# Performance work log

Hardware: AMD Instinct MI355X
Metric: run time of the kernel (lower is better)

Reference implementation:

```python
import jax, jax.numpy as jnp
import numpy as np

B, SQ, SK, D = 8, 4096, 4096, 64


def setup_inputs() -> dict:
    key = jax.random.key(0)
    k1, k2, k3 = jax.random.split(key, 3)
    x1 = jax.random.normal(k1, (B, SQ, D), dtype=jnp.float32)   # queries
    x2 = jax.random.normal(k2, (B, SK, D), dtype=jnp.float32)   # keys
    x3 = jax.random.normal(k3, (B, SK, D), dtype=jnp.float32)   # values
    x4 = 0                                                      # dropout p (static, 0 => deterministic)
    x5 = jnp.ones((1,), dtype=jnp.float32)                      # scale divisor
    return {"x1": x1, "x2": x2, "x3": x3, "x4": x4, "x5": x5}


def reference(x1, x2, x3, x4, x5):
    # scores: [B, Sq, Sk]
    scores = jnp.einsum("bqd,bkd->bqk", x1, x2) / x5
    attn = jax.nn.softmax(scores, axis=-1)
    p = float(x4)  # static python scalar
    if p > 0.0:
        mask = jax.random.bernoulli(jax.random.key(42), 1.0 - p, attn.shape)
        attn = attn * mask.astype(attn.dtype) / (1.0 - p)
    # out: [B, Sq, D]
    return jnp.einsum("bqk,bkd->bqd", attn, x3)
```

## Files before the change

kernel.cpp:

```cpp
#include <hip/hip_runtime.h>


typedef _Float16 f16x8 __attribute__((ext_vector_type(8)));
typedef _Float16 f16x4 __attribute__((ext_vector_type(4)));
typedef __fp16   h16x2 __attribute__((ext_vector_type(2)));
typedef float    f32x4 __attribute__((ext_vector_type(4)));
typedef float    f32x16 __attribute__((ext_vector_type(16)));

constexpr int kB  = 8;
constexpr int kSQ = 4096;
constexpr int kSK = 4096;
constexpr int kD  = 64;
constexpr int KSPLIT = 4;
constexpr int SKH = kSK / KSPLIT;
constexpr int BQ  = 128;
constexpr int MT  = 2;
constexpr int BK  = 64;
constexpr int PSTR = 72;
constexpr float kLog2e = 1.44269504088896340736f;
constexpr float kDeferThr = 11.5f;

static __device__ __forceinline__ f16x4 pack4(float a, float b, float c, float d) {
    h16x2 p0 = __builtin_amdgcn_cvt_pkrtz(a, b);
    h16x2 p1 = __builtin_amdgcn_cvt_pkrtz(c, d);
    f16x4 r;
    r[0] = (_Float16)p0[0]; r[1] = (_Float16)p0[1];
    r[2] = (_Float16)p1[0]; r[3] = (_Float16)p1[1];
    return r;
}
static __device__ __forceinline__ f16x8 pack8(const float4& a, const float4& c) {
    f16x4 lo = pack4(a.x, a.y, a.z, a.w);
    f16x4 hi = pack4(c.x, c.y, c.z, c.w);
    f16x8 f;
    f[0] = lo[0]; f[1] = lo[1]; f[2] = lo[2]; f[3] = lo[3];
    f[4] = hi[0]; f[5] = hi[1]; f[6] = hi[2]; f[7] = hi[3];
    return f;
}
static __device__ __forceinline__ unsigned pkrtz_u(float a, float b) {
    union { h16x2 h; unsigned u; } cv;
    cv.h = __builtin_amdgcn_cvt_pkrtz(a, b);
    return cv.u;
}
static __device__ __forceinline__ float xhalf_max(float x) {
    union { float f; unsigned u; } uv; uv.f = x;
    auto pr = __builtin_amdgcn_permlane32_swap(uv.u, uv.u, false, false);
    union { unsigned u; float f; } r0, r1;
    r0.u = pr[0]; r1.u = pr[1];
    return fmaxf(r0.f, r1.f);
}

typedef const __attribute__((address_space(1))) unsigned int* gu32p;
typedef __attribute__((address_space(3))) unsigned int* lu32p;
static __device__ __forceinline__ void gload_lds16(const void* g, void* l) {
    __builtin_amdgcn_global_load_lds((gu32p)g, (lu32p)l, 16, 0, 0);
}

#define PA_SLICE(dst, sv, rb) do {                                          \
    unsigned c0 = pkrtz_u((sv)[(rb)+0], (sv)[(rb)+1]);                      \
    unsigned c1 = pkrtz_u((sv)[(rb)+2], (sv)[(rb)+3]);                      \
    unsigned c2 = pkrtz_u((sv)[(rb)+4], (sv)[(rb)+5]);                      \
    unsigned c3 = pkrtz_u((sv)[(rb)+6], (sv)[(rb)+7]);                      \
    auto r02 = __builtin_amdgcn_permlane32_swap(c0, c2, false, false);      \
    auto r13 = __builtin_amdgcn_permlane32_swap(c1, c3, false, false);      \
    union { unsigned u[4]; f16x8 v; } _r;                                   \
    _r.u[0] = r02[0]; _r.u[1] = r13[0]; _r.u[2] = r02[1]; _r.u[3] = r13[1]; \
    dst = _r.v;                                                             \
} while (0)

__global__ __launch_bounds__(256, 2)
void fattn_prepass(const float* __restrict__ Kg,
                   const float* __restrict__ Vg,
                   _Float16* __restrict__ Kh,
                   _Float16* __restrict__ Vt)
{
    __shared__ _Float16 tr[kD][BK];

    const int tid = threadIdx.x;
    const int kt  = blockIdx.x;
    const int b   = blockIdx.y;

    const int k = tid >> 2;
    const int p = tid & 3;
    const int gk = kt * BK + k;

    {
        const float* src = Kg + ((size_t)b * kSK + gk) * kD + p * 16;
        const float4 a0 = *(const float4*)(src + 0);
        const float4 a1 = *(const float4*)(src + 4);
        const float4 a2 = *(const float4*)(src + 8);
        const float4 a3 = *(const float4*)(src + 12);
        _Float16* dst = Kh + ((size_t)b * kSK + gk) * kD;
        const int fb0 = 2 * p, fb1 = 2 * p + 1;
        *(f16x8*)&dst[(fb0 ^ (gk & 7)) * 8] = pack8(a0, a1);
        *(f16x8*)&dst[(fb1 ^ (gk & 7)) * 8] = pack8(a2, a3);
    }
    {
        const float* src = Vg + ((size_t)b * kSK + gk) * kD + p * 16;
        const float4 a0 = *(const float4*)(src + 0);
        const float4 a1 = *(const float4*)(src + 4);
        const float4 a2 = *(const float4*)(src + 8);
        const float4 a3 = *(const float4*)(src + 12);
        const float v[16] = {a0.x,a0.y,a0.z,a0.w, a1.x,a1.y,a1.z,a1.w,
                             a2.x,a2.y,a2.z,a2.w, a3.x,a3.y,a3.z,a3.w};
#pragma unroll
        for (int j = 0; j < 16; ++j)
            tr[p * 16 + j][k] = (_Float16)v[j];
    }
    __syncthreads();
    {
        const int f  = tid >> 2;
        const int p2 = tid & 3;
        const f16x8 b0 = *(const f16x8*)&tr[f][p2 * 16 + 0];
        const f16x8 b1 = *(const f16x8*)&tr[f][p2 * 16 + 8];
        _Float16* dst = Vt + (((size_t)b * 64 + kt) * kD + f) * BK;
        const int kb0 = 2 * p2, kb1 = 2 * p2 + 1;
        *(f16x8*)&dst[(kb0 ^ (f & 7)) * 8] = b0;
        *(f16x8*)&dst[(kb1 ^ (f & 7)) * 8] = b1;
    }
}

__global__ __launch_bounds__(512, 2)
void fattn_fused(const float* __restrict__ Qg,
                 const _Float16* __restrict__ Kh,
                 const _Float16* __restrict__ Vt,
                 const float* __restrict__ sdiv,
                 float* __restrict__ Og)
{
    __shared__ __align__(16) char smem[131072];
    _Float16* sKb = (_Float16*)smem;
    _Float16* sVb = (_Float16*)(smem + 65536);
    _Float16* sPart = (_Float16*)smem;
    float2*   sMl   = (float2*)(smem + (size_t)2 * 4 * 64 * PSTR * 2);

    const int tid  = threadIdx.x;
    const int w    = tid >> 6;
    const int lane = tid & 63;
    const int l31  = lane & 31;
    const int hi   = lane >> 5;
    const int ks   = w & 3;
    const int mh   = w >> 2;

    const int flat = blockIdx.x;
    const int b    = flat & 7;
    const int qi   = flat >> 3;
    const int qb   = qi * BQ;

    const float qscale = kLog2e / sdiv[0];

    const float* Qb = Qg + ((size_t)b * kSQ + qb) * kD;
    const _Float16* Khb = Kh + ((size_t)b * kSK + (size_t)ks * SKH) * kD;
    const _Float16* Vtb = Vt + (((size_t)b * 64 + (size_t)ks * (SKH / BK)) * kD) * BK;

    _Float16* sK = sKb + (ks * 2) * 4096;
    _Float16* sV = sVb + (ks * 2) * 4096;

    f16x8 qf[MT][4];
#pragma unroll
    for (int mt = 0; mt < MT; ++mt) {
        const float* qrow = Qb + (size_t)(mh * 64 + mt * 32 + l31) * kD;
#pragma unroll
        for (int ds = 0; ds < 4; ++ds) {
            const float4 a  = *(const float4*)(qrow + ds * 16 + hi * 8);
            const float4 cc = *(const float4*)(qrow + ds * 16 + hi * 8 + 4);
            float4 as = make_float4(a.x * qscale, a.y * qscale, a.z * qscale, a.w * qscale);
            float4 cs = make_float4(cc.x * qscale, cc.y * qscale, cc.z * qscale, cc.w * qscale);
            qf[mt][ds] = pack8(as, cs);
        }
    }

    f16x8 ones;
#pragma unroll
    for (int j = 0; j < 8; ++j) ones[j] = (_Float16)1.0f;

    int offA[4];
#pragma unroll
    for (int i = 0; i < 4; ++i)
        offA[i] = l31 * 64 + (((2 * i + hi) ^ (l31 & 7)) * 8);

    auto stage = [&](int kt, int buf) {
        const char* gk = (const char*)(Khb + (size_t)kt * BK * kD) + mh * 4096 + lane * 16;
        const char* gv = (const char*)(Vtb + (size_t)kt * kD * BK) + mh * 4096 + lane * 16;
        char* lk = (char*)&sK[buf * 4096] + mh * 4096;
        char* lv = (char*)&sV[buf * 4096] + mh * 4096;
        gload_lds16(gk,        lk);
        gload_lds16(gk + 1024, lk + 1024);
        gload_lds16(gk + 2048, lk + 2048);
        gload_lds16(gk + 3072, lk + 3072);
        gload_lds16(gv,        lv);
        gload_lds16(gv + 1024, lv + 1024);
        gload_lds16(gv + 2048, lv + 2048);
        gload_lds16(gv + 3072, lv + 3072);
    };

    f32x16 oL[MT], oH[MT];
    f32x16 ol[MT];
    float m_i[MT];
#pragma unroll
    for (int mt = 0; mt < MT; ++mt) {
        m_i[mt] = -1e30f;
#pragma unroll
        for (int r = 0; r < 16; ++r) { oL[mt][r] = 0.0f; oH[mt][r] = 0.0f; ol[mt][r] = 0.0f; }
    }

    stage(0, 0);
    __syncthreads();

    const int nIter = SKH / BK;
    for (int kt = 0; kt < nIter; ++kt) {
        const int buf = kt & 1;
        if (kt + 1 < nIter) stage(kt + 1, buf ^ 1);

        f16x8 kf0[4], kf1[4];
#pragma unroll
        for (int ds = 0; ds < 4; ++ds) {
            kf0[ds] = *(const f16x8*)&sK[buf * 4096 + offA[ds]];
            kf1[ds] = *(const f16x8*)&sK[buf * 4096 + offA[ds] + 2048];
        }

        f32x16 s0[MT], s1[MT];
#pragma unroll
        for (int mt = 0; mt < MT; ++mt)
#pragma unroll
            for (int r = 0; r < 16; ++r) { s0[mt][r] = 0.0f; s1[mt][r] = 0.0f; }

        __builtin_amdgcn_s_setprio(1);
#pragma unroll
        for (int ds = 0; ds < 4; ++ds)
#pragma unroll
            for (int mt = 0; mt < MT; ++mt) {
                s0[mt] = __builtin_amdgcn_mfma_f32_32x32x16_f16(kf0[ds], qf[mt][ds], s0[mt], 0, 0, 0);
                s1[mt] = __builtin_amdgcn_mfma_f32_32x32x16_f16(kf1[ds], qf[mt][ds], s1[mt], 0, 0, 0);
            }
        __builtin_amdgcn_s_setprio(0);

        f16x8 vf[4][2];
#pragma unroll
        for (int s = 0; s < 4; ++s) {
            vf[s][0] = *(const f16x8*)&sV[buf * 4096 + offA[s]];
            vf[s][1] = *(const f16x8*)&sV[buf * 4096 + offA[s] + 2048];
        }

#pragma unroll
        for (int mt = 0; mt < MT; ++mt) {
            float t[16];
#pragma unroll
            for (int r = 0; r < 16; ++r) t[r] = fmaxf(s0[mt][r], s1[mt][r]);
#pragma unroll
            for (int r = 0; r < 8; ++r)  t[r] = fmaxf(t[r], t[r + 8]);
#pragma unroll
            for (int r = 0; r < 4; ++r)  t[r] = fmaxf(t[r], t[r + 4]);
            float rm = fmaxf(fmaxf(t[0], t[1]), fmaxf(t[2], t[3]));
            rm = xhalf_max(rm);

            if (!__all(rm <= m_i[mt] + kDeferThr)) {
                const float mnew  = fmaxf(m_i[mt], rm);
                const float alpha = __builtin_amdgcn_exp2f(m_i[mt] - mnew);
                ol[mt][0] *= alpha;
#pragma unroll
                for (int r = 0; r < 16; ++r) { oL[mt][r] *= alpha; oH[mt][r] *= alpha; }
                m_i[mt] = mnew;
            }

#pragma unroll
            for (int r = 0; r < 16; ++r) {
                s0[mt][r] = __builtin_amdgcn_exp2f(s0[mt][r] - m_i[mt]);
                s1[mt][r] = __builtin_amdgcn_exp2f(s1[mt][r] - m_i[mt]);
            }

            f16x8 pa[4];
            PA_SLICE(pa[0], s0[mt], 0);
            PA_SLICE(pa[1], s0[mt], 8);
            PA_SLICE(pa[2], s1[mt], 0);
            PA_SLICE(pa[3], s1[mt], 8);

            __builtin_amdgcn_s_setprio(1);
#pragma unroll
            for (int s = 0; s < 4; ++s) {
                oL[mt] = __builtin_amdgcn_mfma_f32_32x32x16_f16(vf[s][0], pa[s], oL[mt], 0, 0, 0);
                oH[mt] = __builtin_amdgcn_mfma_f32_32x32x16_f16(vf[s][1], pa[s], oH[mt], 0, 0, 0);
                ol[mt] = __builtin_amdgcn_mfma_f32_32x32x16_f16(ones,     pa[s], ol[mt], 0, 0, 0);
            }
            __builtin_amdgcn_s_setprio(0);
        }

        __syncthreads();
    }

#pragma unroll
    for (int mt = 0; mt < MT; ++mt) {
        const int ql = mt * 32 + l31;
        const float lf = ol[mt][0];
        const float inv = 1.0f / lf;
        _Float16* prow = sPart + ((size_t)(mh * 4 + ks) * 64 + ql) * PSTR;
#pragma unroll
        for (int g = 0; g < 4; ++g) {
            *(f16x4*)&prow[g * 8 + hi * 4] =
                pack4(oL[mt][4 * g] * inv, oL[mt][4 * g + 1] * inv,
                      oL[mt][4 * g + 2] * inv, oL[mt][4 * g + 3] * inv);
            *(f16x4*)&prow[32 + g * 8 + hi * 4] =
                pack4(oH[mt][4 * g] * inv, oH[mt][4 * g + 1] * inv,
                      oH[mt][4 * g + 2] * inv, oH[mt][4 * g + 3] * inv);
        }
        if (hi == 0) sMl[(mh * 4 + ks) * 64 + ql] = make_float2(m_i[mt], lf);
    }
    __syncthreads();

    {
        const int qrow = tid >> 2;
        const int cc   = (tid & 3) * 16;
        const int emh  = qrow >> 6;
        const int eql  = qrow & 63;

        float2 ml[KSPLIT];
        float m = -1e30f;
#pragma unroll
        for (int s = 0; s < KSPLIT; ++s) {
            ml[s] = sMl[(emh * 4 + s) * 64 + eql];
            m = fmaxf(m, ml[s].x);
        }
        float wgt[KSPLIT];
        float lsum = 0.f;
#pragma unroll
        for (int s = 0; s < KSPLIT; ++s) {
            wgt[s] = __builtin_amdgcn_exp2f(ml[s].x - m) * ml[s].y;
            lsum += wgt[s];
        }
        const float inv = 1.0f / lsum;

        float* orow = Og + (((size_t)b * kSQ + qb + qrow)) * kD + cc;
#pragma unroll
        for (int j = 0; j < 4; ++j) {
            float a0 = 0.f, a1 = 0.f, a2 = 0.f, a3 = 0.f;
#pragma unroll
            for (int s = 0; s < KSPLIT; ++s) {
                const f16x4 a = *(const f16x4*)&sPart[((size_t)(emh * 4 + s) * 64 + eql) * PSTR + cc + j * 4];
                a0 += wgt[s] * (float)a[0];
                a1 += wgt[s] * (float)a[1];
                a2 += wgt[s] * (float)a[2];
                a3 += wgt[s] * (float)a[3];
            }
            *(float4*)&orow[j * 4] = make_float4(a0 * inv, a1 * inv, a2 * inv, a3 * inv);
        }
    }
}

extern "C" void kernel_launch(void* const* d_in, const int* in_sizes, int n_in,
                              void* d_out, int out_size, void* d_ws, size_t ws_size,
                              hipStream_t stream) {
    const float* Q    = (const float*)d_in[0];
    const float* K    = (const float*)d_in[1];
    const float* V    = (const float*)d_in[2];
    const float* sdiv = (const float*)d_in[4];
    float* O = (float*)d_out;

    _Float16* Kh  = (_Float16*)d_ws;
    _Float16* Vt  = Kh + (size_t)kB * kSK * kD;

    fattn_prepass<<<dim3(kSK / BK, kB), dim3(256), 0, stream>>>(K, V, Kh, Vt);
    fattn_fused<<<dim3(kB * (kSQ / BQ)), dim3(512), 0, stream>>>(Q, Kh, Vt, sdiv, O);
}
```

Before: 130.9 us.

## Give each wave private K/V LDS tiles and replace block barriers with waitcnt

```diff
diff --git a/kernel.cpp b/kernel.cpp
--- a/kernel.cpp
+++ b/kernel.cpp
@@ -55,6 +55,10 @@
     __builtin_amdgcn_global_load_lds((gu32p)g, (lu32p)l, 16, 0, 0);
 }
 
+#define WAIT_VMCNT8()  asm volatile("s_waitcnt vmcnt(8)" ::: "memory")
+#define WAIT_VMCNT0()  asm volatile("s_waitcnt vmcnt(0)" ::: "memory")
+#define WAIT_LGKM0()   asm volatile("s_waitcnt lgkmcnt(0)" ::: "memory")
+
 #define PA_SLICE(dst, sv, rb) do {                                          \
     unsigned c0 = pkrtz_u((sv)[(rb)+0], (sv)[(rb)+1]);                      \
     unsigned c1 = pkrtz_u((sv)[(rb)+2], (sv)[(rb)+3]);                      \
@@ -119,7 +123,7 @@
     }
 }
 
-__global__ __launch_bounds__(512, 2)
+__global__ __launch_bounds__(512, 1)
 void fattn_fused(const float* __restrict__ Qg,
                  const _Float16* __restrict__ Kh,
                  const _Float16* __restrict__ Vt,
@@ -127,10 +131,6 @@
                  float* __restrict__ Og)
 {
     __shared__ __align__(16) char smem[131072];
-    _Float16* sKb = (_Float16*)smem;
-    _Float16* sVb = (_Float16*)(smem + 65536);
-    _Float16* sPart = (_Float16*)smem;
-    float2*   sMl   = (float2*)(smem + (size_t)2 * 4 * 64 * PSTR * 2);
 
     const int tid  = threadIdx.x;
     const int w    = tid >> 6;
@@ -140,6 +140,11 @@
     const int ks   = w & 3;
     const int mh   = w >> 2;
 
+    _Float16* sK = (_Float16*)(smem + (size_t)w * 8192);
+    _Float16* sV = (_Float16*)(smem + 65536 + (size_t)w * 8192);
+    _Float16* sPart = (_Float16*)smem;
+    float2*   sMl   = (float2*)(smem + (size_t)2 * 4 * 64 * PSTR * 2);
+
     const int flat = blockIdx.x;
     const int b    = flat & 7;
     const int qi   = flat >> 3;
@@ -150,9 +155,6 @@
     const float* Qb = Qg + ((size_t)b * kSQ + qb) * kD;
     const _Float16* Khb = Kh + ((size_t)b * kSK + (size_t)ks * SKH) * kD;
     const _Float16* Vtb = Vt + (((size_t)b * 64 + (size_t)ks * (SKH / BK)) * kD) * BK;
-
-    _Float16* sK = sKb + (ks * 2) * 4096;
-    _Float16* sV = sVb + (ks * 2) * 4096;
 
     f16x8 qf[MT][4];
 #pragma unroll
@@ -177,19 +179,19 @@
     for (int i = 0; i < 4; ++i)
         offA[i] = l31 * 64 + (((2 * i + hi) ^ (l31 & 7)) * 8);
 
-    auto stage = [&](int kt, int buf) {
-        const char* gk = (const char*)(Khb + (size_t)kt * BK * kD) + mh * 4096 + lane * 16;
-        const char* gv = (const char*)(Vtb + (size_t)kt * kD * BK) + mh * 4096 + lane * 16;
-        char* lk = (char*)&sK[buf * 4096] + mh * 4096;
-        char* lv = (char*)&sV[buf * 4096] + mh * 4096;
-        gload_lds16(gk,        lk);
-        gload_lds16(gk + 1024, lk + 1024);
-        gload_lds16(gk + 2048, lk + 2048);
-        gload_lds16(gk + 3072, lk + 3072);
-        gload_lds16(gv,        lv);
-        gload_lds16(gv + 1024, lv + 1024);
-        gload_lds16(gv + 2048, lv + 2048);
-        gload_lds16(gv + 3072, lv + 3072);
+    auto stageK = [&](int kt) {
+        const char* gk = (const char*)(Khb + (size_t)kt * BK * kD) + lane * 16;
+        char* lk = (char*)sK + lane * 16;
+#pragma unroll
+        for (int i = 0; i < 8; ++i)
+            gload_lds16(gk + i * 1024, lk + i * 1024);
+    };
+    auto stageV = [&](int kt) {
+        const char* gv = (const char*)(Vtb + (size_t)kt * kD * BK) + lane * 16;
+        char* lv = (char*)sV + lane * 16;
+#pragma unroll
+        for (int i = 0; i < 8; ++i)
+            gload_lds16(gv + i * 1024, lv + i * 1024);
     };
 
     f32x16 oL[MT], oH[MT];
@@ -202,20 +204,22 @@
         for (int r = 0; r < 16; ++r) { oL[mt][r] = 0.0f; oH[mt][r] = 0.0f; ol[mt][r] = 0.0f; }
     }
 
-    stage(0, 0);
-    __syncthreads();
+    stageK(0);
+    stageV(0);
 
     const int nIter = SKH / BK;
     for (int kt = 0; kt < nIter; ++kt) {
-        const int buf = kt & 1;
-        if (kt + 1 < nIter) stage(kt + 1, buf ^ 1);
-
+        const bool more = (kt + 1 < nIter);
+
+        WAIT_VMCNT8();
         f16x8 kf0[4], kf1[4];
 #pragma unroll
         for (int ds = 0; ds < 4; ++ds) {
-            kf0[ds] = *(const f16x8*)&sK[buf * 4096 + offA[ds]];
-            kf1[ds] = *(const f16x8*)&sK[buf * 4096 + offA[ds] + 2048];
-        }
+            kf0[ds] = *(const f16x8*)&sK[offA[ds]];
+            kf1[ds] = *(const f16x8*)&sK[offA[ds] + 2048];
+        }
+        WAIT_LGKM0();
+        if (more) stageK(kt + 1);
 
         f32x16 s0[MT], s1[MT];
 #pragma unroll
@@ -233,11 +237,12 @@
             }
         __builtin_amdgcn_s_setprio(0);
 
+        if (more) { WAIT_VMCNT8(); } else { WAIT_VMCNT0(); }
         f16x8 vf[4][2];
 #pragma unroll
         for (int s = 0; s < 4; ++s) {
-            vf[s][0] = *(const f16x8*)&sV[buf * 4096 + offA[s]];
-            vf[s][1] = *(const f16x8*)&sV[buf * 4096 + offA[s] + 2048];
+            vf[s][0] = *(const f16x8*)&sV[offA[s]];
+            vf[s][1] = *(const f16x8*)&sV[offA[s] + 2048];
         }
 
 #pragma unroll
@@ -283,9 +288,11 @@
             __builtin_amdgcn_s_setprio(0);
         }
 
-        __syncthreads();
-    }
-
+        WAIT_LGKM0();
+        if (more) stageV(kt + 1);
+    }
+
+    __syncthreads();
 #pragma unroll
     for (int mt = 0; mt < MT; ++mt) {
         const int ql = mt * 32 + l31;
```

New measurement: 134.5 us. +2.8%, slower.
